# Kernel optimization log

Hardware: AMD Instinct MI355X
Metric: run time of the kernel (lower is better)

## Reference

```python
import jax, jax.numpy as jnp
import numpy as np

N_NODES = 50000
N_EDGES = 800000
DIM = 128
BN_EPS = 1e-5
GATE_EPS = 1e-6


def setup_inputs() -> dict:
    key = jax.random.key(0)
    ks = jax.random.split(key, 14)
    scale = 1.0 / np.sqrt(DIM)
    inp = {
        "h": jax.random.normal(ks[0], (N_NODES, DIM), dtype=jnp.float32),
        "e": jax.random.normal(ks[1], (N_EDGES, DIM), dtype=jnp.float32),
        "src": jax.random.randint(ks[2], (N_EDGES,), 0, N_NODES),
        "dst": jax.random.randint(ks[3], (N_EDGES,), 0, N_NODES),
        # Linear A, B, D, E (n_mlp_layer=1 -> single Linear each)
        "Wa": jax.random.uniform(ks[4], (DIM, DIM), jnp.float32, -scale, scale),
        "ba": jax.random.uniform(ks[5], (DIM,), jnp.float32, -scale, scale),
        "Wb": jax.random.uniform(ks[6], (DIM, DIM), jnp.float32, -scale, scale),
        "bb": jax.random.uniform(ks[7], (DIM,), jnp.float32, -scale, scale),
        "Wd": jax.random.uniform(ks[8], (DIM, DIM), jnp.float32, -scale, scale),
        "bd": jax.random.uniform(ks[9], (DIM,), jnp.float32, -scale, scale),
        "We": jax.random.uniform(ks[10], (DIM, DIM), jnp.float32, -scale, scale),
        "be": jax.random.uniform(ks[11], (DIM,), jnp.float32, -scale, scale),
        # BatchNorm1d affine params (fresh init: gamma=1, beta=0)
        "gamma": jnp.ones((DIM,), jnp.float32),
        "beta": jnp.zeros((DIM,), jnp.float32),
    }
    return inp


def reference(h, e, src, dst, Wa, ba, Wb, bb, Wd, bd, We, be, gamma, beta):
    N = h.shape[0]
    # dense node projections
    Ah = h @ Wa + ba
    Bh = h @ Wb + bb
    Dh = h @ Wd + bd
    Eh = h @ We + be
    # edge gather + sigmoid gate: e_ij = Dh[src] + Eh[dst]
    sigma = jax.nn.sigmoid(Dh[src] + Eh[dst])          # [E, D]
    # scatter-sum by destination node (variable degree)
    num = jax.ops.segment_sum(sigma * Bh[src], dst, num_segments=N)
    den = jax.ops.segment_sum(sigma, dst, num_segments=N) + GATE_EPS
    h_new = Ah + num / den
    # BatchNorm1d (training mode: biased batch statistics) + relu
    mean = jnp.mean(h_new, axis=0)
    var = jnp.mean(jnp.square(h_new - mean), axis=0)
    h_new = (h_new - mean) * jax.lax.rsqrt(var + BN_EPS) * gamma + beta
    h_new = jax.nn.relu(h_new)
    # residual=False (default), dropout=0.0 -> identity
    return h_new, e
```

## Files before the change

kernel.cpp:

```cpp
#include <hip/hip_runtime.h>
#include <hip/hip_bf16.h>

#define DIM 128
#define GATE_EPS 1e-6f
#define BN_EPS 1e-5f

typedef unsigned int u32;
typedef unsigned short u16;

__device__ __forceinline__ float bflo(u32 u) { return __uint_as_float(u << 16); }
__device__ __forceinline__ float bfhi(u32 u) { return __uint_as_float(u & 0xffff0000u); }

__device__ __forceinline__ u16 f2bf(float f) {
    u32 u = __float_as_uint(f);
    u32 r = (u + 0x7fffu + ((u >> 16) & 1u)) >> 16;
    return (u16)r;
}

__device__ __forceinline__ float loadF(const void* p, size_t i, int bf) {
    if (bf) return __uint_as_float(((u32)((const u16*)p)[i]) << 16);
    return ((const float*)p)[i];
}

__global__ void detect_dtype(const void* __restrict__ h, int* __restrict__ flag) {
    if (threadIdx.x == 0 && blockIdx.x == 0) {
        const u16* us = (const u16*)h;
        int cnt = 0;
        for (int i = 0; i < 256; ++i) {
            int e8 = (us[2 * i] >> 7) & 0xFF;
            if (e8 >= 0x60 && e8 <= 0x8F) ++cnt;
        }
        *flag = (cnt >= 192) ? 1 : 0;
    }
}

__global__ __launch_bounds__(256) void proj_gemm(
    const void* __restrict__ h,
    const void* __restrict__ W0, const void* __restrict__ b0,
    const void* __restrict__ W1, const void* __restrict__ b1,
    const void* __restrict__ W2, const void* __restrict__ b2,
    const void* __restrict__ W3, const void* __restrict__ b3,
    float* __restrict__ oAh, u32* __restrict__ oDB, u32* __restrict__ oEhb,
    int N, const int* __restrict__ flagp)
{
    const void* W; const void* bias;
    switch (blockIdx.y) {
        case 0:  W = W0; bias = b0; break;
        case 1:  W = W1; bias = b1; break;
        case 2:  W = W2; bias = b2; break;
        default: W = W3; bias = b3; break;
    }
    const int bf = *flagp;

    __shared__ float Hs[64][DIM + 4];
    __shared__ float Ws[16][DIM];

    const int t  = threadIdx.x;
    const int m0 = blockIdx.x * 64;

    if (bf) {
        for (int f = t; f < 1024; f += 256) {
            int r = f >> 4, c8 = f & 15;
            int gr = m0 + r;
            uint4 v = make_uint4(0u, 0u, 0u, 0u);
            if (gr < N) v = ((const uint4*)h)[(size_t)gr * 16 + c8];
            float* p = &Hs[r][c8 * 8];
            p[0] = bflo(v.x); p[1] = bfhi(v.x);
            p[2] = bflo(v.y); p[3] = bfhi(v.y);
            p[4] = bflo(v.z); p[5] = bfhi(v.z);
            p[6] = bflo(v.w); p[7] = bfhi(v.w);
        }
    } else {
        for (int f = t; f < 2048; f += 256) {
            int r = f >> 5, c4 = f & 31;
            int gr = m0 + r;
            float4 v = make_float4(0.f, 0.f, 0.f, 0.f);
            if (gr < N) v = ((const float4*)h)[(size_t)gr * 32 + c4];
            float* p = &Hs[r][c4 * 4];
            p[0] = v.x; p[1] = v.y; p[2] = v.z; p[3] = v.w;
        }
    }

    const int cg = t & 31;
    const int rg = t >> 5;

    float acc[8][4];
    #pragma unroll
    for (int i = 0; i < 8; ++i)
        #pragma unroll
        for (int j = 0; j < 4; ++j) acc[i][j] = 0.f;

    for (int kc = 0; kc < DIM; kc += 16) {
        __syncthreads();
        if (bf) {
            int r = t >> 4, c8 = t & 15;
            uint4 v = ((const uint4*)W)[(size_t)(kc + r) * 16 + c8];
            float* p = &Ws[r][c8 * 8];
            p[0] = bflo(v.x); p[1] = bfhi(v.x);
            p[2] = bflo(v.y); p[3] = bfhi(v.y);
            p[4] = bflo(v.z); p[5] = bfhi(v.z);
            p[6] = bflo(v.w); p[7] = bfhi(v.w);
        } else {
            for (int f = t; f < 512; f += 256) {
                int r = f >> 5, c4 = f & 31;
                float4 v = ((const float4*)W)[(size_t)(kc + r) * 32 + c4];
                float* p = &Ws[r][c4 * 4];
                p[0] = v.x; p[1] = v.y; p[2] = v.z; p[3] = v.w;
            }
        }
        __syncthreads();
        #pragma unroll
        for (int kk = 0; kk < 16; ++kk) {
            float4 w = *((const float4*)&Ws[kk][cg * 4]);
            #pragma unroll
            for (int i = 0; i < 8; ++i) {
                float hv = Hs[rg * 8 + i][kc + kk];
                acc[i][0] += hv * w.x;
                acc[i][1] += hv * w.y;
                acc[i][2] += hv * w.z;
                acc[i][3] += hv * w.w;
            }
        }
    }

    float bv[4];
    #pragma unroll
    for (int j = 0; j < 4; ++j) bv[j] = loadF(bias, cg * 4 + j, bf);

    const int y = blockIdx.y;
    #pragma unroll
    for (int i = 0; i < 8; ++i) {
        int gr = m0 + rg * 8 + i;
        if (gr < N) {
            float v0 = acc[i][0] + bv[0];
            float v1 = acc[i][1] + bv[1];
            float v2 = acc[i][2] + bv[2];
            float v3 = acc[i][3] + bv[3];
            if (y == 0) {
                ((float4*)oAh)[(size_t)gr * 32 + cg] = make_float4(v0, v1, v2, v3);
            } else {
                uint2 p;
                p.x = (u32)f2bf(v0) | ((u32)f2bf(v1) << 16);
                p.y = (u32)f2bf(v2) | ((u32)f2bf(v3) << 16);
                size_t idx;
                if (y == 1)      idx = (size_t)gr * 64 + 32 + cg;
                else if (y == 2) idx = (size_t)gr * 64 + cg;
                else             idx = (size_t)gr * 32 + cg;
                u32* base = (y == 3) ? oEhb : oDB;
                ((uint2*)base)[idx] = p;
            }
        }
    }
}

__global__ __launch_bounds__(256) void k_hist(const int* __restrict__ dst,
                                              int* __restrict__ deg, int E)
{
    int e = blockIdx.x * 256 + threadIdx.x;
    if (e < E) atomicAdd(&deg[dst[e]], 1);
}

__global__ __launch_bounds__(256) void k_scan1(const int* __restrict__ deg,
                                               int* __restrict__ rowstart,
                                               int* __restrict__ part, int N)
{
    __shared__ int s[256];
    int t = threadIdx.x;
    int i = blockIdx.x * 256 + t;
    int d = (i < N) ? deg[i] : 0;
    s[t] = d;
    __syncthreads();
    for (int off = 1; off < 256; off <<= 1) {
        int v = (t >= off) ? s[t - off] : 0;
        __syncthreads();
        s[t] += v;
        __syncthreads();
    }
    if (i < N) rowstart[i] = s[t] - d;
    if (t == 255) part[blockIdx.x] = s[255];
}

__global__ void k_scan2(int* __restrict__ part, int nb)
{
    __shared__ int s[256];
    int t = threadIdx.x;
    int d = (t < nb) ? part[t] : 0;
    s[t] = d;
    __syncthreads();
    for (int off = 1; off < 256; off <<= 1) {
        int v = (t >= off) ? s[t - off] : 0;
        __syncthreads();
        s[t] += v;
        __syncthreads();
    }
    if (t < nb) part[t] = s[t] - d;
}

__global__ __launch_bounds__(256) void k_scan3(int* __restrict__ rowstart,
                                               int* __restrict__ cursor,
                                               const int* __restrict__ part,
                                               int N, int E)
{
    int i = blockIdx.x * 256 + threadIdx.x;
    if (i < N) {
        int v = rowstart[i] + part[blockIdx.x];
        rowstart[i] = v;
        cursor[i] = v;
    }
    if (i == 0) rowstart[N] = E;
}

__global__ __launch_bounds__(256) void k_scatter(const int* __restrict__ src,
                                                 const int* __restrict__ dst,
                                                 int* __restrict__ cursor,
                                                 int* __restrict__ esrc, int E)
{
    int e = blockIdx.x * 256 + threadIdx.x;
    if (e < E) {
        int pos = atomicAdd(&cursor[dst[e]], 1);
        esrc[pos] = src[e];
    }
}

__global__ __launch_bounds__(256) void k_aggregate(
    const float* __restrict__ Ah, const u32* __restrict__ DB,
    const u32* __restrict__ Ehb,
    const int* __restrict__ rowstart, const int* __restrict__ esrc,
    float* __restrict__ hnew, float* __restrict__ gsum, float* __restrict__ gsq,
    int N)
{
    int t = threadIdx.x;
    int lane = t & 63;
    int wv = t >> 6;
    int nquads = (N + 3) >> 2;

    float lsum0 = 0.f, lsum1 = 0.f, lsq0 = 0.f, lsq1 = 0.f;
    for (int q = blockIdx.x; q < nquads; q += gridDim.x) {
        int n = q * 4 + wv;
        if (n < N) {
            u32 ehp = Ehb[(size_t)n * 64 + lane];
            float eh0 = bflo(ehp), eh1 = bfhi(ehp);
            float2 ahp = ((const float2*)Ah)[(size_t)n * 64 + lane];
            float num0 = 0.f, den0 = 0.f, num1 = 0.f, den1 = 0.f;
            int beg = rowstart[n], end = rowstart[n + 1];
            for (int k = beg; k < end; ++k) {
                int s = esrc[k];
                u32 dhp = DB[(size_t)s * 128 + lane];
                u32 bhp = DB[(size_t)s * 128 + 64 + lane];
                float sg0 = 1.f / (1.f + __expf(-(bflo(dhp) + eh0)));
                float sg1 = 1.f / (1.f + __expf(-(bfhi(dhp) + eh1)));
                num0 = fmaf(sg0, bflo(bhp), num0); den0 += sg0;
                num1 = fmaf(sg1, bfhi(bhp), num1); den1 += sg1;
            }
            float x0 = ahp.x + num0 / (den0 + GATE_EPS);
            float x1 = ahp.y + num1 / (den1 + GATE_EPS);
            ((float2*)hnew)[(size_t)n * 64 + lane] = make_float2(x0, x1);
            lsum0 += x0; lsq0 += x0 * x0;
            lsum1 += x1; lsq1 += x1 * x1;
        }
    }
    __shared__ float S0[256], S1[256], Q0[256], Q1[256];
    S0[t] = lsum0; S1[t] = lsum1; Q0[t] = lsq0; Q1[t] = lsq1;
    __syncthreads();
    if (t < 64) {
        float s0 = S0[t] + S0[t + 64] + S0[t + 128] + S0[t + 192];
        float s1 = S1[t] + S1[t + 64] + S1[t + 128] + S1[t + 192];
        float q0 = Q0[t] + Q0[t + 64] + Q0[t + 128] + Q0[t + 192];
        float q1 = Q1[t] + Q1[t + 64] + Q1[t + 128] + Q1[t + 192];
        atomicAdd(&gsum[2 * t],     s0);
        atomicAdd(&gsum[2 * t + 1], s1);
        atomicAdd(&gsq[2 * t],      q0);
        atomicAdd(&gsq[2 * t + 1],  q1);
    }
}

__global__ void bn_finalize(const float* __restrict__ gsum, const float* __restrict__ gsq,
                            const void* __restrict__ gamma, const void* __restrict__ beta,
                            float* __restrict__ scale, float* __restrict__ shift,
                            int N, const int* __restrict__ flagp)
{
    int c = threadIdx.x;
    int bf = *flagp;
    if (c < DIM) {
        float invn = 1.f / (float)N;
        float mean = gsum[c] * invn;
        float var  = gsq[c] * invn - mean * mean;
        float g = loadF(gamma, c, bf);
        float b = loadF(beta, c, bf);
        float sc = rsqrtf(var + BN_EPS) * g;
        scale[c] = sc;
        shift[c] = b - mean * sc;
    }
}

__global__ __launch_bounds__(256) void bn_apply(
    const float* __restrict__ hnew, const float* __restrict__ scale,
    const float* __restrict__ shift, void* __restrict__ outh,
    int total, const int* __restrict__ flagp)
{
    __shared__ float s_sc[DIM], s_sh[DIM];
    int t = threadIdx.x;
    if (t < DIM) { s_sc[t] = scale[t]; s_sh[t] = shift[t]; }
    __syncthreads();
    int bf = *flagp;

    int idx = blockIdx.x * 256 + t;
    int stride = gridDim.x * 256;
    for (int i = idx; i < total; i += stride) {
        int c = i & 127;
        float x = fmaxf(0.f, hnew[i] * s_sc[c] + s_sh[c]);
        if (bf) ((u16*)outh)[i] = f2bf(x);
        else    ((float*)outh)[i] = x;
    }
}

__global__ __launch_bounds__(256) void copy_e(
    const void* __restrict__ e, void* __restrict__ dout,
    size_t nd, size_t ecount, const int* __restrict__ flagp)
{
    int bf = *flagp;
    size_t esz = bf ? 2 : 4;
    const uint4* s = (const uint4*)e;
    uint4* d = (uint4*)((char*)dout + nd * esz);
    size_t n16 = (ecount * esz) / 16;
    size_t idx = (size_t)blockIdx.x * 256 + threadIdx.x;
    size_t stride = (size_t)gridDim.x * 256;
    for (size_t i = idx; i < n16; i += stride) d[i] = s[i];
}

extern "C" void kernel_launch(void* const* d_in, const int* in_sizes, int n_in,
                              void* d_out, int out_size, void* d_ws, size_t ws_size,
                              hipStream_t stream)
{
    const void* h     = d_in[0];
    const void* e     = d_in[1];
    const int*  src   = (const int*)d_in[2];
    const int*  dst   = (const int*)d_in[3];
    const void* Wa    = d_in[4];
    const void* ba    = d_in[5];
    const void* Wb    = d_in[6];
    const void* bb    = d_in[7];
    const void* Wd    = d_in[8];
    const void* bd    = d_in[9];
    const void* We    = d_in[10];
    const void* be    = d_in[11];
    const void* gamma = d_in[12];
    const void* beta  = d_in[13];

    const int N = in_sizes[0] / DIM;
    const int E = in_sizes[2];
    const size_t nd = (size_t)N * DIM;
    const size_t ecount = (size_t)E * DIM;

    float* ws    = (float*)d_ws;
    float* Ah    = ws;
    float* hnew  = ws + nd;
    u32*   DB    = (u32*)(ws + 2 * nd);
    u32*   Ehb   = (u32*)(ws + 3 * nd);
    float* gsum  = ws + 3 * nd + nd / 2;
    float* gsq   = gsum + DIM;
    float* scale = gsum + 2 * DIM;
    float* shift = gsum + 3 * DIM;
    int*   flag  = (int*)(gsum + 4 * DIM);
    int*   deg      = flag + 64;
    int*   rowstart = deg + N;
    int*   cursor   = rowstart + N + 1;
    int*   part     = cursor + N;
    int*   esrc     = part + 256;

    detect_dtype<<<1, 64, 0, stream>>>(h, flag);

    hipMemsetAsync(gsum, 0, 4 * DIM * sizeof(float), stream);
    hipMemsetAsync(deg, 0, (size_t)N * sizeof(int), stream);

    const int nbE = (E + 255) / 256;
    const int nbN = (N + 255) / 256;

    k_hist<<<nbE, 256, 0, stream>>>(dst, deg, E);
    k_scan1<<<nbN, 256, 0, stream>>>(deg, rowstart, part, N);
    k_scan2<<<1, 256, 0, stream>>>(part, nbN);
    k_scan3<<<nbN, 256, 0, stream>>>(rowstart, cursor, part, N, E);
    k_scatter<<<nbE, 256, 0, stream>>>(src, dst, cursor, esrc, E);

    dim3 g1((N + 63) / 64, 4);
    proj_gemm<<<g1, 256, 0, stream>>>(h, Wa, ba, Wb, bb, Wd, bd, We, be,
                                      Ah, DB, Ehb, N, flag);

    k_aggregate<<<2048, 256, 0, stream>>>(Ah, DB, Ehb, rowstart, esrc,
                                          hnew, gsum, gsq, N);

    bn_finalize<<<1, 128, 0, stream>>>(gsum, gsq, gamma, beta, scale, shift, N, flag);

    bn_apply<<<2048, 256, 0, stream>>>(hnew, scale, shift, d_out, (int)nd, flag);

    copy_e<<<4096, 256, 0, stream>>>(e, d_out, nd, ecount, flag);
}
```

Before: 559.7 us.

## Interleave D and B projections per lane and unroll edge gather by four

The projection GEMM now writes the bf16 Dh and Bh values interleaved so that each lane fetches its Dh pair and Bh pair with a single 8-byte load per edge. The aggregation loop is unrolled four edges at a time so that more independent gathers are in flight. It also clamps the BN variance at zero and moves the memsets ahead of dtype detection, widening the first memset to cover the flag. The interleaved writes are 4-byte strided stores from two separate blocks, which may make the GEMM epilogue less efficient.

```diff
diff --git a/kernel.cpp b/kernel.cpp
--- a/kernel.cpp
+++ b/kernel.cpp
@@ -138,16 +138,17 @@
             float v3 = acc[i][3] + bv[3];
             if (y == 0) {
                 ((float4*)oAh)[(size_t)gr * 32 + cg] = make_float4(v0, v1, v2, v3);
-            } else {
+            } else if (y == 3) {
                 uint2 p;
                 p.x = (u32)f2bf(v0) | ((u32)f2bf(v1) << 16);
                 p.y = (u32)f2bf(v2) | ((u32)f2bf(v3) << 16);
-                size_t idx;
-                if (y == 1)      idx = (size_t)gr * 64 + 32 + cg;
-                else if (y == 2) idx = (size_t)gr * 64 + cg;
-                else             idx = (size_t)gr * 32 + cg;
-                u32* base = (y == 3) ? oEhb : oDB;
-                ((uint2*)base)[idx] = p;
+                ((uint2*)oEhb)[(size_t)gr * 32 + cg] = p;
+            } else {
+                u32 px = (u32)f2bf(v0) | ((u32)f2bf(v1) << 16);
+                u32 py = (u32)f2bf(v2) | ((u32)f2bf(v3) << 16);
+                u32* dbp = oDB + (size_t)gr * 128 + 4 * cg;
+                if (y == 2) { dbp[0] = px; dbp[2] = py; }
+                else        { dbp[1] = px; dbp[3] = py; }
             }
         }
     }
@@ -233,6 +234,7 @@
     int lane = t & 63;
     int wv = t >> 6;
     int nquads = (N + 3) >> 2;
+    const uint2* DB2 = (const uint2*)DB;
 
     float lsum0 = 0.f, lsum1 = 0.f, lsq0 = 0.f, lsq1 = 0.f;
     for (int q = blockIdx.x; q < nquads; q += gridDim.x) {
@@ -243,14 +245,37 @@
             float2 ahp = ((const float2*)Ah)[(size_t)n * 64 + lane];
             float num0 = 0.f, den0 = 0.f, num1 = 0.f, den1 = 0.f;
             int beg = rowstart[n], end = rowstart[n + 1];
-            for (int k = beg; k < end; ++k) {
-                int s = esrc[k];
-                u32 dhp = DB[(size_t)s * 128 + lane];
-                u32 bhp = DB[(size_t)s * 128 + 64 + lane];
-                float sg0 = 1.f / (1.f + __expf(-(bflo(dhp) + eh0)));
-                float sg1 = 1.f / (1.f + __expf(-(bfhi(dhp) + eh1)));
-                num0 = fmaf(sg0, bflo(bhp), num0); den0 += sg0;
-                num1 = fmaf(sg1, bfhi(bhp), num1); den1 += sg1;
+            int k = beg;
+            for (; k + 4 <= end; k += 4) {
+                int s0 = esrc[k], s1 = esrc[k + 1], s2 = esrc[k + 2], s3 = esrc[k + 3];
+                uint2 dA = DB2[(size_t)s0 * 64 + lane];
+                uint2 dB = DB2[(size_t)s1 * 64 + lane];
+                uint2 dC = DB2[(size_t)s2 * 64 + lane];
+                uint2 dD = DB2[(size_t)s3 * 64 + lane];
+                float sA0 = 1.f / (1.f + __expf(-(bflo(dA.x) + eh0)));
+                float sA1 = 1.f / (1.f + __expf(-(bfhi(dA.x) + eh1)));
+                float sB0 = 1.f / (1.f + __expf(-(bflo(dB.x) + eh0)));
+                float sB1 = 1.f / (1.f + __expf(-(bfhi(dB.x) + eh1)));
+                float sC0 = 1.f / (1.f + __expf(-(bflo(dC.x) + eh0)));
+                float sC1 = 1.f / (1.f + __expf(-(bfhi(dC.x) + eh1)));
+                float sD0 = 1.f / (1.f + __expf(-(bflo(dD.x) + eh0)));
+                float sD1 = 1.f / (1.f + __expf(-(bfhi(dD.x) + eh1)));
+                num0 = fmaf(sA0, bflo(dA.y), num0); den0 += sA0;
+                num1 = fmaf(sA1, bfhi(dA.y), num1); den1 += sA1;
+                num0 = fmaf(sB0, bflo(dB.y), num0); den0 += sB0;
+                num1 = fmaf(sB1, bfhi(dB.y), num1); den1 += sB1;
+                num0 = fmaf(sC0, bflo(dC.y), num0); den0 += sC0;
+                num1 = fmaf(sC1, bfhi(dC.y), num1); den1 += sC1;
+                num0 = fmaf(sD0, bflo(dD.y), num0); den0 += sD0;
+                num1 = fmaf(sD1, bfhi(dD.y), num1); den1 += sD1;
+            }
+            for (; k < end; ++k) {
+                int s0 = esrc[k];
+                uint2 dA = DB2[(size_t)s0 * 64 + lane];
+                float sa0 = 1.f / (1.f + __expf(-(bflo(dA.x) + eh0)));
+                float sa1 = 1.f / (1.f + __expf(-(bfhi(dA.x) + eh1)));
+                num0 = fmaf(sa0, bflo(dA.y), num0); den0 += sa0;
+                num1 = fmaf(sa1, bfhi(dA.y), num1); den1 += sa1;
             }
             float x0 = ahp.x + num0 / (den0 + GATE_EPS);
             float x1 = ahp.y + num1 / (den1 + GATE_EPS);
@@ -284,7 +309,7 @@
     if (c < DIM) {
         float invn = 1.f / (float)N;
         float mean = gsum[c] * invn;
-        float var  = gsq[c] * invn - mean * mean;
+        float var  = fmaxf(gsq[c] * invn - mean * mean, 0.f);
         float g = loadF(gamma, c, bf);
         float b = loadF(beta, c, bf);
         float sc = rsqrtf(var + BN_EPS) * g;
@@ -368,10 +393,10 @@
     int*   part     = cursor + N;
     int*   esrc     = part + 256;
 
+    hipMemsetAsync(gsum, 0, (4 * DIM + 64) * sizeof(float), stream);
+    hipMemsetAsync(deg, 0, (size_t)N * sizeof(int), stream);
+
     detect_dtype<<<1, 64, 0, stream>>>(h, flag);
-
-    hipMemsetAsync(gsum, 0, 4 * DIM * sizeof(float), stream);
-    hipMemsetAsync(deg, 0, (size_t)N * sizeof(int), stream);
 
     const int nbE = (E + 255) / 256;
     const int nbN = (N + 255) / 256;
```

New measurement: 548.4 us. 2.0% less time.
